# Kernel optimization log

Measured on AMD Instinct MI355X. Metric: run time of the kernel, lower is better.

## Reference

```python
import jax, jax.numpy as jnp
import numpy as np

SCALE_FACTOR = 1.0
VIS_MAX = 1024


def setup_inputs() -> dict:
    key = jax.random.key(0)
    kq, kk, kv = jax.random.split(key, 3)
    B, C, H, W = 4, 256, 64, 64
    Q = jax.random.normal(kq, (B, C, H, W), dtype=jnp.float32)
    K = jax.random.normal(kk, (B, C, H, W), dtype=jnp.float32)
    V = jax.random.normal(kv, (B, C, H, W), dtype=jnp.float32)
    return {"Q": Q, "K": K, "V": V}


def reference(Q, K, V):
    # Q,K: [B,C,H,W] -> flatten spatial dims to HW
    B, C, H, W = Q.shape
    HW = H * W
    Q_flat = Q.reshape(B, C, HW).transpose(0, 2, 1)  # [B, HW, C]
    K_flat = K.reshape(B, C, HW)                      # [B, C, HW]
    # Full scaled score matrix [B, HW, HW]; argmax over keys reproduces the
    # chunked running-max/argmax (strict '>' update keeps first max, matching
    # jnp.argmax tie-breaking).
    S = jnp.einsum('bqc,bck->bqk', Q_flat, K_flat) * SCALE_FACTOR
    H_idx = jnp.argmax(S, axis=2).astype(jnp.int64)   # [B, HW]
    vis = min(VIS_MAX, HW)
    S_vis = S[:, :vis, :vis]                          # [B, vis, vis]
    return S_vis, H_idx
```

## Files before the change

kernel.cpp:

```cpp
#include <hip/hip_runtime.h>
#include <stdint.h>

#define B_   4
#define C_   256
#define HW_  4096
#define VIS_ 1024
#define KE_  768

using half8   = __attribute__((ext_vector_type(8))) _Float16;
using floatx4 = __attribute__((ext_vector_type(4))) float;

__device__ __forceinline__ unsigned mapf(float v) {
    unsigned u = __float_as_uint(v);
    return (u & 0x80000000u) ? ~u : (u | 0x80000000u);
}

__global__ void init_ws_kernel(unsigned long long* ws, int n) {
    int i = blockIdx.x * blockDim.x + threadIdx.x;
    if (i < n) ws[i] = 0ull;
}

__global__ void finalize_kernel(const unsigned long long* __restrict__ ws,
                                float* __restrict__ out1, int n) {
    int i = blockIdx.x * blockDim.x + threadIdx.x;
    if (i < n) {
        unsigned kinv = (unsigned)(ws[i] & 0xFFFFFFFFull);
        out1[i] = (float)(HW_ - 1 - (int)kinv);
    }
}


__global__ __launch_bounds__(256) void split_transpose_kernel(
    const float* __restrict__ Q, const float* __restrict__ K,
    _Float16* __restrict__ Aexp, _Float16* __restrict__ Bexp)
{
    __shared__ float tile[64][65];
    const int hw0 = blockIdx.x * 64;
    const int c0  = blockIdx.y * 64;
    const int z = blockIdx.z, b = z >> 1, which = z & 1;
    const float* src = (which ? K : Q) + (size_t)b * C_ * HW_;
    _Float16* dst = (which ? Bexp : Aexp) + (size_t)b * HW_ * KE_;
    const int t = threadIdx.x;

    #pragma unroll
    for (int i = 0; i < 4; ++i) {
        int c  = (t >> 4) + i * 16;
        int hw = (t & 15) * 4;
        float4 v = *(const float4*)(src + (size_t)(c0 + c) * HW_ + hw0 + hw);
        tile[c][hw] = v.x; tile[c][hw+1] = v.y; tile[c][hw+2] = v.z; tile[c][hw+3] = v.w;
    }
    __syncthreads();

    #pragma unroll
    for (int i = 0; i < 2; ++i) {
        int id  = t + i * 256;
        int row = id >> 3;
        int c8  = (id & 7) * 8;
        half8 h8, l8;
        #pragma unroll
        for (int j = 0; j < 8; ++j) {
            float v = tile[c8 + j][row];
            _Float16 h = (_Float16)v;
            h8[j] = h;
            l8[j] = (_Float16)(v - (float)h);
        }
        _Float16* base = dst + (size_t)(hw0 + row) * KE_ + c0 + c8;
        *(half8*)(base + 0 * C_) = h8;
        *(half8*)(base + 1 * C_) = which ? l8 : h8;
        *(half8*)(base + 2 * C_) = which ? h8 : l8;
    }
}

__device__ __forceinline__ void gl2lds16(const _Float16* g, _Float16* l) {
    __builtin_amdgcn_global_load_lds(
        (const __attribute__((address_space(1))) void*)g,
        (__attribute__((address_space(3))) void*)l, 16, 0, 0);
}

__global__ __launch_bounds__(256, 2) void gemm_mfma_kernel(
    const _Float16* __restrict__ Aexp, const _Float16* __restrict__ Bexp,
    float* __restrict__ out0, unsigned long long* __restrict__ keys)
{
    __shared__ __align__(16) _Float16 Al[128 * 32];
    __shared__ __align__(16) _Float16 Bl[128 * 32];
    __shared__ unsigned long long red2[128][2];

    const int t    = threadIdx.x;
    const int lane = t & 63;
    const int wave = t >> 6;
    const int quad = lane >> 4;
    const int s    = lane & 15;
    const int wm   = (wave >> 1) * 64;
    const int wn   = (wave & 1) * 64;
    const int kt = blockIdx.x, qt = blockIdx.y, b = blockIdx.z;

    const _Float16* Ab = Aexp + (size_t)b * HW_ * KE_ + (size_t)(qt * 128) * KE_;
    const _Float16* Bb = Bexp + (size_t)b * HW_ * KE_ + (size_t)(kt * 128) * KE_;

    const int ca = t, cb = t + 256;
    const int ra = ca >> 2, oa = (ca & 3) * 8;
    const int rb = cb >> 2, ob = (cb & 3) * 8;

    floatx4 acc[4][4] = {};

    for (int it = 0; it < KE_ / 32; ++it) {
        const int k0 = it * 32;
        gl2lds16(Ab + (size_t)ra * KE_ + k0 + oa, Al + ca * 8);
        gl2lds16(Ab + (size_t)rb * KE_ + k0 + ob, Al + cb * 8);
        gl2lds16(Bb + (size_t)ra * KE_ + k0 + oa, Bl + ca * 8);
        gl2lds16(Bb + (size_t)rb * KE_ + k0 + ob, Bl + cb * 8);
        __syncthreads();

        half8 a[4], bf[4];
        #pragma unroll
        for (int mi = 0; mi < 4; ++mi)
            a[mi] = *(half8*)(Al + (wm + mi * 16 + s) * 32 + quad * 8);
        #pragma unroll
        for (int ni = 0; ni < 4; ++ni)
            bf[ni] = *(half8*)(Bl + (wn + ni * 16 + s) * 32 + quad * 8);
        #pragma unroll
        for (int mi = 0; mi < 4; ++mi)
            #pragma unroll
            for (int ni = 0; ni < 4; ++ni)
                acc[mi][ni] = __builtin_amdgcn_mfma_f32_16x16x32_f16(a[mi], bf[ni], acc[mi][ni], 0, 0, 0);
        __syncthreads();
    }

    if (qt < 8 && kt < 8) {
        #pragma unroll
        for (int mi = 0; mi < 4; ++mi)
            #pragma unroll
            for (int r = 0; r < 4; ++r) {
                int grow = qt * 128 + wm + mi * 16 + quad * 4 + r;
                float* orow = out0 + ((size_t)b * VIS_ + grow) * VIS_ + kt * 128;
                #pragma unroll
                for (int ni = 0; ni < 4; ++ni)
                    orow[wn + ni * 16 + s] = acc[mi][ni][r];
            }
    }

    #pragma unroll
    for (int mi = 0; mi < 4; ++mi) {
        #pragma unroll
        for (int r = 0; r < 4; ++r) {
            float best = acc[mi][0][r];
            int bcol = wn + s;
            #pragma unroll
            for (int ni = 1; ni < 4; ++ni) {
                float v = acc[mi][ni][r];
                if (v > best) { best = v; bcol = wn + ni * 16 + s; }
            }
            int gcol = kt * 128 + bcol;
            unsigned long long key = ((unsigned long long)mapf(best) << 32)
                                   | (unsigned)(HW_ - 1 - gcol);
            #pragma unroll
            for (int m = 1; m < 16; m <<= 1) {
                unsigned long long o = __shfl_xor(key, m, 64);
                if (o > key) key = o;
            }
            if (s == 0) red2[wm + mi * 16 + quad * 4 + r][wave & 1] = key;
        }
    }
    __syncthreads();
    if (t < 128) {
        unsigned long long k0v = red2[t][0], k1v = red2[t][1];
        unsigned long long kk = k0v > k1v ? k0v : k1v;
        atomicMax(&keys[(size_t)b * HW_ + qt * 128 + t], kk);
    }
}

#define BT   64
#define BK   32
#define LDP  68

__global__ __launch_bounds__(256) void gemm_argmax_kernel(
    const float* __restrict__ Q, const float* __restrict__ K,
    float* __restrict__ out0, unsigned long long* __restrict__ ws)
{
    __shared__ float As[BK][LDP];
    __shared__ float Bs[BK][LDP];
    __shared__ unsigned long long red[BT][17];

    const int t  = threadIdx.x;
    const int tx = t & 15;
    const int ty = t >> 4;
    const int k0 = blockIdx.x * BT;
    const int q0 = blockIdx.y * BT;
    const int b  = blockIdx.z;

    const float* Qb = Q + (size_t)b * C_ * HW_;
    const float* Kb = K + (size_t)b * C_ * HW_;

    float acc[4][4] = {{0.f},{0.f},{0.f},{0.f}};

    for (int c0 = 0; c0 < C_; c0 += BK) {
        #pragma unroll
        for (int i = 0; i < 2; ++i) {
            int idx = i * 256 + t;
            int row = idx >> 4;
            int col = (idx & 15) * 4;
            const float4 a  = *(const float4*)(Qb + (size_t)(c0 + row) * HW_ + q0 + col);
            const float4 bv = *(const float4*)(Kb + (size_t)(c0 + row) * HW_ + k0 + col);
            *(float4*)(&As[row][col]) = a;
            *(float4*)(&Bs[row][col]) = bv;
        }
        __syncthreads();
        #pragma unroll
        for (int cc = 0; cc < BK; ++cc) {
            const float4 av = *(const float4*)(&As[cc][ty * 4]);
            const float4 bv = *(const float4*)(&Bs[cc][tx * 4]);
            const float a_[4] = {av.x, av.y, av.z, av.w};
            const float b_[4] = {bv.x, bv.y, bv.z, bv.w};
            #pragma unroll
            for (int i = 0; i < 4; ++i)
                #pragma unroll
                for (int j = 0; j < 4; ++j)
                    acc[i][j] = fmaf(a_[i], b_[j], acc[i][j]);
        }
        __syncthreads();
    }

    if (q0 < VIS_ && k0 < VIS_) {
        #pragma unroll
        for (int i = 0; i < 4; ++i) {
            float4 v = make_float4(acc[i][0], acc[i][1], acc[i][2], acc[i][3]);
            size_t off = (size_t)b * VIS_ * VIS_ + (size_t)(q0 + ty * 4 + i) * VIS_ + (k0 + tx * 4);
            *(float4*)(out0 + off) = v;
        }
    }

    #pragma unroll
    for (int i = 0; i < 4; ++i) {
        float best = acc[i][0];
        int   bj   = 0;
        #pragma unroll
        for (int j = 1; j < 4; ++j)
            if (acc[i][j] > best) { best = acc[i][j]; bj = j; }
        int kidx = k0 + tx * 4 + bj;
        unsigned long long key = ((unsigned long long)mapf(best) << 32)
                               | (unsigned)(HW_ - 1 - kidx);
        red[ty * 4 + i][tx] = key;
    }
    __syncthreads();
    if (t < BT) {
        unsigned long long best = red[t][0];
        #pragma unroll
        for (int j = 1; j < 16; ++j) {
            unsigned long long v = red[t][j];
            if (v > best) best = v;
        }
        atomicMax(&ws[(size_t)b * HW_ + q0 + t], best);
    }
}

extern "C" void kernel_launch(void* const* d_in, const int* in_sizes, int n_in,
                              void* d_out, int out_size, void* d_ws, size_t ws_size,
                              hipStream_t stream) {
    const float* Q = (const float*)d_in[0];
    const float* K = (const float*)d_in[1];
    float* out0 = (float*)d_out;
    float* out1 = out0 + (size_t)B_ * VIS_ * VIS_;

    unsigned long long* keys = (unsigned long long*)d_ws;
    const size_t keys_bytes = (size_t)B_ * HW_ * 8;
    const size_t exp_elems  = (size_t)B_ * HW_ * KE_;
    const size_t need = keys_bytes + 2 * exp_elems * sizeof(_Float16);

    const int n = B_ * HW_;
    init_ws_kernel<<<(n + 255) / 256, 256, 0, stream>>>(keys, n);

    if (ws_size >= need) {
        _Float16* Aexp = (_Float16*)((char*)d_ws + keys_bytes);
        _Float16* Bexp = Aexp + exp_elems;
        split_transpose_kernel<<<dim3(HW_ / 64, C_ / 64, 2 * B_), 256, 0, stream>>>(Q, K, Aexp, Bexp);
        gemm_mfma_kernel<<<dim3(HW_ / 128, HW_ / 128, B_), 256, 0, stream>>>(Aexp, Bexp, out0, keys);
    } else {
        gemm_argmax_kernel<<<dim3(HW_ / BT, HW_ / BT, B_), 256, 0, stream>>>(Q, K, out0, keys);
    }

    finalize_kernel<<<(n + 255) / 256, 256, 0, stream>>>(keys, out1, n);
}
```

Baseline: 231.0 us.

## Rewrite MFMA GEMM as 256x256 tile, 8-wave, multi-buffered LDS pipeline

The fp16-split MFMA GEMM moves from a 128x128 tile with 4 waves to a 256x256 tile with 8 waves. Global-to-LDS loads go through an 8-slot LDS ring with an XOR swizzle to avoid bank conflicts, and explicit vmcnt/lgkmcnt waits, barriers and setprio interleave loading with MFMA issue. The aim is to hide global-load latency and raise arithmetic intensity per byte loaded. In exchange it uses 128KB of LDS and more accumulator registers, runs one block per CU, and launches only 1024 blocks.

```diff
diff --git a/kernel.cpp b/kernel.cpp
--- a/kernel.cpp
+++ b/kernel.cpp
@@ -77,80 +77,198 @@
         (__attribute__((address_space(3))) void*)l, 16, 0, 0);
 }
 
-__global__ __launch_bounds__(256, 2) void gemm_mfma_kernel(
+
+#define BARRIER __builtin_amdgcn_s_barrier()
+#define LGKM0   asm volatile("s_waitcnt lgkmcnt(0)" ::: "memory")
+#define VMC(n)  asm volatile("s_waitcnt vmcnt(" #n ")" ::: "memory")
+#define SCHEDB  __builtin_amdgcn_sched_barrier(0)
+
+__device__ __forceinline__ void stage_half(const _Float16* __restrict__ g,
+                                           _Float16* lb, int t, int kbase)
+{
+    #pragma unroll
+    for (int j = 0; j < 2; ++j) {
+        const int c   = t + j * 512;
+        const int row = c >> 2;
+        const int ch  = (c & 3) ^ ((row >> 1) & 3);
+        gl2lds16(g + (size_t)row * KE_ + kbase + ch * 8, lb + c * 8);
+    }
+}
+
+template<int DB, int KH, int MQ>
+__device__ __forceinline__ void ds_load_a(const _Float16* lds, int wave_m, int s,
+                                          int quad, half8 (&a)[4]) {
+    const _Float16* base = lds + (DB * 4 + KH) * 8192;
+    #pragma unroll
+    for (int mi = 0; mi < 4; ++mi) {
+        int row = wave_m * 128 + MQ * 64 + mi * 16 + s;
+        int ch  = quad ^ ((row >> 1) & 3);
+        a[mi] = *(const half8*)(base + row * 32 + ch * 8);
+    }
+}
+
+template<int DB, int KH>
+__device__ __forceinline__ void ds_load_b(const _Float16* lds, int wave_n, int s,
+                                          int quad, half8 (&bfr)[4]) {
+    const _Float16* base = lds + (DB * 4 + 2 + KH) * 8192;
+    #pragma unroll
+    for (int ni = 0; ni < 4; ++ni) {
+        int col = wave_n * 64 + ni * 16 + s;
+        int ch  = quad ^ ((col >> 1) & 3);
+        bfr[ni] = *(const half8*)(base + col * 32 + ch * 8);
+    }
+}
+
+template<int MQ>
+__device__ __forceinline__ void do_mfma(const half8 (&a)[4], const half8 (&bfr)[4],
+                                        floatx4 (&acc)[8][4]) {
+    __builtin_amdgcn_s_setprio(1);
+    #pragma unroll
+    for (int mi = 0; mi < 4; ++mi)
+        #pragma unroll
+        for (int ni = 0; ni < 4; ++ni)
+            acc[MQ * 4 + mi][ni] = __builtin_amdgcn_mfma_f32_16x16x32_f16(
+                a[mi], bfr[ni], acc[MQ * 4 + mi][ni], 0, 0, 0);
+    __builtin_amdgcn_s_setprio(0);
+}
+
+__global__ __launch_bounds__(512, 1) void gemm_mfma_kernel(
     const _Float16* __restrict__ Aexp, const _Float16* __restrict__ Bexp,
     float* __restrict__ out0, unsigned long long* __restrict__ keys)
 {
-    __shared__ __align__(16) _Float16 Al[128 * 32];
-    __shared__ __align__(16) _Float16 Bl[128 * 32];
-    __shared__ unsigned long long red2[128][2];
-
-    const int t    = threadIdx.x;
-    const int lane = t & 63;
-    const int wave = t >> 6;
-    const int quad = lane >> 4;
-    const int s    = lane & 15;
-    const int wm   = (wave >> 1) * 64;
-    const int wn   = (wave & 1) * 64;
+    __shared__ __align__(16) _Float16 lds[65536];
+
+    const int t      = threadIdx.x;
+    const int lane   = t & 63;
+    const int wave   = t >> 6;
+    const int quad   = lane >> 4;
+    const int s      = lane & 15;
+    const int wave_m = wave >> 2;
+    const int wave_n = wave & 3;
     const int kt = blockIdx.x, qt = blockIdx.y, b = blockIdx.z;
 
-    const _Float16* Ab = Aexp + (size_t)b * HW_ * KE_ + (size_t)(qt * 128) * KE_;
-    const _Float16* Bb = Bexp + (size_t)b * HW_ * KE_ + (size_t)(kt * 128) * KE_;
-
-    const int ca = t, cb = t + 256;
-    const int ra = ca >> 2, oa = (ca & 3) * 8;
-    const int rb = cb >> 2, ob = (cb & 3) * 8;
-
-    floatx4 acc[4][4] = {};
-
-    for (int it = 0; it < KE_ / 32; ++it) {
-        const int k0 = it * 32;
-        gl2lds16(Ab + (size_t)ra * KE_ + k0 + oa, Al + ca * 8);
-        gl2lds16(Ab + (size_t)rb * KE_ + k0 + ob, Al + cb * 8);
-        gl2lds16(Bb + (size_t)ra * KE_ + k0 + oa, Bl + ca * 8);
-        gl2lds16(Bb + (size_t)rb * KE_ + k0 + ob, Bl + cb * 8);
-        __syncthreads();
-
-        half8 a[4], bf[4];
-        #pragma unroll
-        for (int mi = 0; mi < 4; ++mi)
-            a[mi] = *(half8*)(Al + (wm + mi * 16 + s) * 32 + quad * 8);
-        #pragma unroll
-        for (int ni = 0; ni < 4; ++ni)
-            bf[ni] = *(half8*)(Bl + (wn + ni * 16 + s) * 32 + quad * 8);
-        #pragma unroll
-        for (int mi = 0; mi < 4; ++mi)
-            #pragma unroll
-            for (int ni = 0; ni < 4; ++ni)
-                acc[mi][ni] = __builtin_amdgcn_mfma_f32_16x16x32_f16(a[mi], bf[ni], acc[mi][ni], 0, 0, 0);
-        __syncthreads();
-    }
-
-    if (qt < 8 && kt < 8) {
-        #pragma unroll
-        for (int mi = 0; mi < 4; ++mi)
+    const _Float16* Agl = Aexp + (size_t)b * HW_ * KE_ + (size_t)(qt * 256) * KE_;
+    const _Float16* Bgl = Bexp + (size_t)b * HW_ * KE_ + (size_t)(kt * 256) * KE_;
+
+    stage_half(Agl, lds + 0 * 8192, t, 0);
+    stage_half(Bgl, lds + 2 * 8192, t, 0);
+    stage_half(Agl, lds + 1 * 8192, t, 32);
+    stage_half(Bgl, lds + 3 * 8192, t, 32);
+    stage_half(Agl, lds + 4 * 8192, t, 64);
+    stage_half(Bgl, lds + 6 * 8192, t, 64);
+    VMC(4);
+    BARRIER; SCHEDB;
+
+    half8 a[4], bfr[4];
+    floatx4 acc[8][4] = {};
+
+    #pragma unroll 1
+    for (int it = 0; it < 5; ++it) {
+        const int kb1 = (2 * it + 1) * 64;
+        const int kb2 = kb1 + 64;
+        const int kb3 = kb1 + 128;
+        ds_load_a<0, 0, 0>(lds, wave_m, s, quad, a);
+        ds_load_b<0, 0>(lds, wave_n, s, quad, bfr);
+        stage_half(Agl, lds + 5 * 8192, t, kb1 + 32);
+        BARRIER; LGKM0;
+        do_mfma<0>(a, bfr, acc);
+        BARRIER;
+        ds_load_a<0, 0, 1>(lds, wave_m, s, quad, a);
+        stage_half(Bgl, lds + 7 * 8192, t, kb1 + 32);
+        BARRIER; LGKM0;
+        do_mfma<1>(a, bfr, acc);
+        BARRIER;
+        ds_load_a<0, 1, 0>(lds, wave_m, s, quad, a);
+        ds_load_b<0, 1>(lds, wave_n, s, quad, bfr);
+        stage_half(Agl, lds + 0 * 8192, t, kb2);
+        BARRIER; LGKM0;
+        do_mfma<0>(a, bfr, acc);
+        BARRIER;
+        ds_load_a<0, 1, 1>(lds, wave_m, s, quad, a);
+        stage_half(Bgl, lds + 2 * 8192, t, kb2);
+        BARRIER; LGKM0;
+        do_mfma<1>(a, bfr, acc);
+        VMC(4);
+        BARRIER; SCHEDB;
+        ds_load_a<1, 0, 0>(lds, wave_m, s, quad, a);
+        ds_load_b<1, 0>(lds, wave_n, s, quad, bfr);
+        stage_half(Agl, lds + 1 * 8192, t, kb2 + 32);
+        BARRIER; LGKM0;
+        do_mfma<0>(a, bfr, acc);
+        BARRIER;
+        ds_load_a<1, 0, 1>(lds, wave_m, s, quad, a);
+        stage_half(Bgl, lds + 3 * 8192, t, kb2 + 32);
+        BARRIER; LGKM0;
+        do_mfma<1>(a, bfr, acc);
+        BARRIER;
+        ds_load_a<1, 1, 0>(lds, wave_m, s, quad, a);
+        ds_load_b<1, 1>(lds, wave_n, s, quad, bfr);
+        stage_half(Agl, lds + 4 * 8192, t, kb3);
+        BARRIER; LGKM0;
+        do_mfma<0>(a, bfr, acc);
+        BARRIER;
+        ds_load_a<1, 1, 1>(lds, wave_m, s, quad, a);
+        stage_half(Bgl, lds + 6 * 8192, t, kb3);
+        BARRIER; LGKM0;
+        do_mfma<1>(a, bfr, acc);
+        VMC(4);
+        BARRIER; SCHEDB;
+    }
+
+    stage_half(Agl, lds + 5 * 8192, t, 736);
+    stage_half(Bgl, lds + 7 * 8192, t, 736);
+    VMC(0);
+    __syncthreads();
+
+    ds_load_a<0, 0, 0>(lds, wave_m, s, quad, a);
+    ds_load_b<0, 0>(lds, wave_n, s, quad, bfr);
+    do_mfma<0>(a, bfr, acc);
+    ds_load_a<0, 0, 1>(lds, wave_m, s, quad, a);
+    do_mfma<1>(a, bfr, acc);
+    ds_load_a<0, 1, 0>(lds, wave_m, s, quad, a);
+    ds_load_b<0, 1>(lds, wave_n, s, quad, bfr);
+    do_mfma<0>(a, bfr, acc);
+    ds_load_a<0, 1, 1>(lds, wave_m, s, quad, a);
+    do_mfma<1>(a, bfr, acc);
+    ds_load_a<1, 0, 0>(lds, wave_m, s, quad, a);
+    ds_load_b<1, 0>(lds, wave_n, s, quad, bfr);
+    do_mfma<0>(a, bfr, acc);
+    ds_load_a<1, 0, 1>(lds, wave_m, s, quad, a);
+    do_mfma<1>(a, bfr, acc);
+    ds_load_a<1, 1, 0>(lds, wave_m, s, quad, a);
+    ds_load_b<1, 1>(lds, wave_n, s, quad, bfr);
+    do_mfma<0>(a, bfr, acc);
+    ds_load_a<1, 1, 1>(lds, wave_m, s, quad, a);
+    do_mfma<1>(a, bfr, acc);
+
+    if (qt < 4 && kt < 4) {
+        #pragma unroll
+        for (int mi8 = 0; mi8 < 8; ++mi8)
             #pragma unroll
             for (int r = 0; r < 4; ++r) {
-                int grow = qt * 128 + wm + mi * 16 + quad * 4 + r;
-                float* orow = out0 + ((size_t)b * VIS_ + grow) * VIS_ + kt * 128;
+                int grow = qt * 256 + wave_m * 128 + mi8 * 16 + quad * 4 + r;
+                float* orow = out0 + ((size_t)b * VIS_ + grow) * VIS_ + kt * 256 + wave_n * 64;
                 #pragma unroll
                 for (int ni = 0; ni < 4; ++ni)
-                    orow[wn + ni * 16 + s] = acc[mi][ni][r];
+                    orow[ni * 16 + s] = acc[mi8][ni][r];
             }
     }
 
-    #pragma unroll
-    for (int mi = 0; mi < 4; ++mi) {
+    __syncthreads();
+    unsigned long long* red = (unsigned long long*)lds;
+
+    #pragma unroll
+    for (int mi8 = 0; mi8 < 8; ++mi8) {
         #pragma unroll
         for (int r = 0; r < 4; ++r) {
-            float best = acc[mi][0][r];
-            int bcol = wn + s;
+            float best = acc[mi8][0][r];
+            int bcol = wave_n * 64 + s;
             #pragma unroll
             for (int ni = 1; ni < 4; ++ni) {
-                float v = acc[mi][ni][r];
-                if (v > best) { best = v; bcol = wn + ni * 16 + s; }
+                float v = acc[mi8][ni][r];
+                if (v > best) { best = v; bcol = wave_n * 64 + ni * 16 + s; }
             }
-            int gcol = kt * 128 + bcol;
+            int gcol = kt * 256 + bcol;
             unsigned long long key = ((unsigned long long)mapf(best) << 32)
                                    | (unsigned)(HW_ - 1 - gcol);
             #pragma unroll
@@ -158,14 +276,17 @@
                 unsigned long long o = __shfl_xor(key, m, 64);
                 if (o > key) key = o;
             }
-            if (s == 0) red2[wm + mi * 16 + quad * 4 + r][wave & 1] = key;
+            if (s == 0)
+                red[(wave_m * 128 + mi8 * 16 + quad * 4 + r) * 4 + wave_n] = key;
         }
     }
     __syncthreads();
-    if (t < 128) {
-        unsigned long long k0v = red2[t][0], k1v = red2[t][1];
-        unsigned long long kk = k0v > k1v ? k0v : k1v;
-        atomicMax(&keys[(size_t)b * HW_ + qt * 128 + t], kk);
+    if (t < 256) {
+        const unsigned long long* rr = red + t * 4;
+        unsigned long long k0 = rr[0], k1 = rr[1], k2 = rr[2], k3 = rr[3];
+        unsigned long long m01 = k0 > k1 ? k0 : k1;
+        unsigned long long m23 = k2 > k3 ? k2 : k3;
+        atomicMax(&keys[(size_t)b * HW_ + qt * 256 + t], m01 > m23 ? m01 : m23);
     }
 }
 
@@ -273,7 +394,7 @@
         _Float16* Aexp = (_Float16*)((char*)d_ws + keys_bytes);
         _Float16* Bexp = Aexp + exp_elems;
         split_transpose_kernel<<<dim3(HW_ / 64, C_ / 64, 2 * B_), 256, 0, stream>>>(Q, K, Aexp, Bexp);
-        gemm_mfma_kernel<<<dim3(HW_ / 128, HW_ / 128, B_), 256, 0, stream>>>(Aexp, Bexp, out0, keys);
+        gemm_mfma_kernel<<<dim3(HW_ / 256, HW_ / 256, B_), 512, 0, stream>>>(Aexp, Bexp, out0, keys);
     } else {
         gemm_argmax_kernel<<<dim3(HW_ / BT, HW_ / BT, B_), 256, 0, stream>>>(Q, K, out0, keys);
     }
```

Measured after the change: 224.3 us. 1.03x faster.
